# Kernel tuning notes

Measured on AMD Instinct MI355X. Metric: run time of the kernel, lower is better.

## Reference

```python
import jax, jax.numpy as jnp
import numpy as np

BIN_AGG = 16  # binAgg in source
K = 3         # forward-default im2col/col2im kernel size


def _im2col(x, k):
    # torch Im2Col (unfold), pad=0, stride=1, dilation=1
    B, C, H, W = x.shape
    oh, ow = H - k + 1, W - k + 1
    patches = [x[:, :, i:i + oh, j:j + ow] for i in range(k) for j in range(k)]
    cols = jnp.stack(patches, axis=2)            # [B, C, k*k, oh, ow]
    return cols.reshape(B, C * k * k, oh * ow)   # [B, C*k*k, L]


def _col2im(cols, k, H, W):
    # torch Col2Im (fold): overlap-add of patches back to [B, C, H, W]
    B, CK, L = cols.shape
    C = CK // (k * k)
    oh = H - k + 1
    cols = cols.reshape(B, C, k, k, oh, oh)
    img = jnp.zeros((B, C, H, W), cols.dtype)
    for i in range(k):
        for j in range(k):
            img = img.at[:, :, i:i + oh, j:j + oh].add(cols[:, :, i, j])
    return img


def bin_active(x):
    # sign(x) scaled by block-wise mean of |x| over blocks of 16 along last dim
    B, Kd, L = x.shape
    blocks = jnp.abs(x).reshape(B, Kd, L // BIN_AGG, BIN_AGG)
    scale = jnp.mean(blocks, axis=-1, keepdims=True)
    scale = jnp.broadcast_to(scale, blocks.shape).reshape(B, Kd, L)
    return scale * jnp.sign(x)


def setup_inputs() -> dict:
    key = jax.random.key(0)
    ks = jax.random.split(key, 5)
    B, Cin, Cout, H = 8, 64, 128, 130
    x = jax.random.normal(ks[0], (B, Cin, H, H), jnp.float32)
    gamma = 1.0 + 0.1 * jax.random.normal(ks[1], (Cin,), jnp.float32)
    beta = 0.1 * jax.random.normal(ks[2], (Cin,), jnp.float32)
    conv_w = 0.05 * jax.random.normal(ks[3], (Cout, Cin, 3, 3), jnp.float32)
    conv_b = 0.05 * jax.random.normal(ks[4], (Cout,), jnp.float32)
    return {"x": x, "gamma": gamma, "beta": beta, "conv_w": conv_w, "conv_b": conv_b}


def reference(x, gamma, beta, conv_w, conv_b):
    eps = 1e-4  # BatchNorm2d eps in source
    # BatchNorm2d (training-mode batch statistics, affine)
    mean = jnp.mean(x, axis=(0, 2, 3), keepdims=True)
    var = jnp.var(x, axis=(0, 2, 3), keepdims=True)
    xbn = (x - mean) * jax.lax.rsqrt(var + eps) * gamma[None, :, None, None] + beta[None, :, None, None]
    H = x.shape[2]
    cols = _im2col(xbn, K)          # [B, C*9, (H-2)^2]
    cols = bin_active(cols)         # block-mean binary quantization
    img = _col2im(cols, K, H, H)    # [B, C, H, W]
    y = jax.lax.conv_general_dilated(
        img, conv_w, window_strides=(1, 1), padding=((1, 1), (1, 1)),
        dimension_numbers=("NCHW", "OIHW", "NCHW"))
    y = y + conv_b[None, :, None, None]
    return jax.nn.relu(y)
```

## Files before the change

### kernel.cpp

```cpp
#include <hip/hip_runtime.h>
#include <math.h>

#define B_    8
#define CIN   64
#define COUT  128
#define H_    130
#define NPIX  (H_*H_)
#define NPX   (B_*NPIX)
#define IMW   132
#define ROWE  (8*IMW*8)

typedef __attribute__((ext_vector_type(8))) short short8;
typedef __attribute__((ext_vector_type(4))) float f32x4;

__device__ __forceinline__ ushort f2bf(float f) {
    uint u = __builtin_bit_cast(uint, f);
    uint r = (u + 0x7FFFu + ((u >> 16) & 1u)) >> 16;
    return (ushort)r;
}

__global__ __launch_bounds__(256) void bn_stage1(
    const float* __restrict__ x, float* __restrict__ part)
{
    const int c = blockIdx.x, b = blockIdx.y, tid = threadIdx.x;
    const float4* p = (const float4*)(x + ((size_t)b*CIN + c)*NPIX);
    float s = 0.f, q = 0.f;
    for (int i = tid; i < NPIX/4; i += 256) {
        float4 v = p[i];
        s += v.x + v.y + v.z + v.w;
        q += v.x*v.x + v.y*v.y + v.z*v.z + v.w*v.w;
    }
    #pragma unroll
    for (int off = 32; off; off >>= 1) { s += __shfl_down(s, off); q += __shfl_down(q, off); }
    __shared__ float ss[4], qq[4];
    if ((tid & 63) == 0) { ss[tid >> 6] = s; qq[tid >> 6] = q; }
    __syncthreads();
    if (tid == 0) {
        s = ss[0] + ss[1] + ss[2] + ss[3];
        q = qq[0] + qq[1] + qq[2] + qq[3];
        part[(c*B_ + b)*2]     = s;
        part[(c*B_ + b)*2 + 1] = q;
    }
}

__global__ void bn_stage2(
    const float* __restrict__ part, const float* __restrict__ gamma,
    const float* __restrict__ beta, float* __restrict__ abuf, float* __restrict__ bbuf)
{
    int c = threadIdx.x;
    float s = 0.f, q = 0.f;
    for (int b = 0; b < B_; ++b) { s += part[(c*B_+b)*2]; q += part[(c*B_+b)*2+1]; }
    float mean = s * (1.0f/135200.f);
    float var  = q * (1.0f/135200.f) - mean*mean;
    float a = gamma[c] / sqrtf(var + 1e-4f);
    abuf[c] = a;
    bbuf[c] = beta[c] - mean * a;
}

__global__ __launch_bounds__(256) void wprep(
    const float* __restrict__ w, ushort* __restrict__ wT)
{
    int i = blockIdx.x*256 + threadIdx.x;
    int co = i / 576, k = i - co*576;
    int dydx = k >> 6, ci = k & 63;
    wT[i] = f2bf(w[co*576 + ci*9 + dydx]);
}

__global__ __launch_bounds__(256) void binfold(
    const float* __restrict__ x, const float* __restrict__ abuf,
    const float* __restrict__ bbuf, ushort* __restrict__ img)
{
    __shared__ __align__(16) ushort tile[H_*66];
    __shared__ float absrow[4][132];
    __shared__ float wsum[4][24];
    const int yy = blockIdx.x;
    const int b  = blockIdx.y;
    const int tid = threadIdx.x, wv = tid >> 6, lane = tid & 63;
    uint* rowU = (uint*)(img + (size_t)(b*IMW + yy)*ROWE);

    if (yy == 0 || yy == IMW-1) {
        for (int i = tid; i < ROWE/2; i += 256) rowU[i] = 0u;
        return;
    }
    const int y = yy - 1;
    const float county = (float)min(min(y + 1, 3), H_ - y);

    for (int it = 0; it < 16; ++it) {
        const int ci = wv*16 + it;
        const float* row = x + (((size_t)b*CIN + ci)*H_ + y)*H_;
        const float a = abuf[ci], bb = bbuf[ci];
        float v0 = a*row[lane]      + bb;
        float v1 = a*row[lane + 64] + bb;
        float v2 = 0.f;
        if (lane < 2) v2 = a*row[lane + 128] + bb;
        absrow[wv][lane]      = fabsf(v0);
        absrow[wv][lane + 64] = fabsf(v1);
        if (lane < 2) absrow[wv][lane + 128] = fabsf(v2);
        asm volatile("s_waitcnt lgkmcnt(0)" ::: "memory");
        if (lane < 24) {
            int j = lane >> 3, bx = lane & 7;
            int s = j + bx*16;
            float acc = 0.f;
            #pragma unroll
            for (int t = 0; t < 16; ++t) acc += absrow[wv][s + t];
            wsum[wv][j*8 + bx] = acc;
        }
        asm volatile("s_waitcnt lgkmcnt(0)" ::: "memory");
        #pragma unroll
        for (int rep = 0; rep < 3; ++rep) {
            int xp = lane + rep*64;
            if (xp < H_) {
                float v = (rep == 0) ? v0 : (rep == 1) ? v1 : v2;
                float sgn = (v > 0.f) ? 1.f : ((v < 0.f) ? -1.f : 0.f);
                float sum = 0.f;
                #pragma unroll
                for (int j = 0; j < 3; ++j) {
                    int ox = xp - j;
                    if ((unsigned)ox < 128u) sum += wsum[wv][j*8 + (ox >> 4)];
                }
                tile[xp*66 + ci] = f2bf(sgn * county * sum * 0.0625f);
            }
        }
    }
    __syncthreads();
    const uint* tU = (const uint*)tile;
    for (int i = tid; i < 8*H_*4; i += 256) {
        int cg = (int)((unsigned)i / 520u);
        int r  = i - cg*520;
        int xp = r >> 2, u = r & 3;
        rowU[(cg*IMW + xp + 1)*4 + u] = tU[xp*33 + cg*4 + u];
    }
    if (tid < 64) {
        int cg = tid >> 3, side = (tid >> 2) & 1, u = tid & 3;
        rowU[(cg*IMW + (side ? (IMW-1) : 0))*4 + u] = 0u;
    }
}

#define LDSE (3*ROWE + 128)
__global__ __launch_bounds__(256, 3) void conv_mfma(
    const ushort* __restrict__ img, const ushort* __restrict__ wT,
    const float* __restrict__ bias, float* __restrict__ out)
{
    __shared__ __align__(16) ushort sB[LDSE];
    const int y = blockIdx.x, b = blockIdx.y;
    const int tid = threadIdx.x, lane = tid & 63, wv = tid >> 6;
    const int l16 = lane & 15, quad = lane >> 4;
    const int ch = wv >> 1, ph = wv & 1;

    {
        const uint4* src = (const uint4*)(img + (size_t)(b*IMW + y)*ROWE);
        uint4* dst = (uint4*)sB;
        for (int i = tid; i < 3*ROWE/8; i += 256) dst[i] = src[i];
    }
    __syncthreads();

    int wIdx[4];
    #pragma unroll
    for (int mt = 0; mt < 4; ++mt)
        wIdx[mt] = (ch*64 + mt*16 + l16)*576 + quad*8;

    const int ldsLane = (quad*IMW + ph*64 + l16)*8;

    f32x4 acc[4][5];
    #pragma unroll
    for (int mt = 0; mt < 4; ++mt)
        #pragma unroll
        for (int nt = 0; nt < 5; ++nt)
            acc[mt][nt] = (f32x4){0.f, 0.f, 0.f, 0.f};

    #pragma unroll 3
    for (int dydx = 0; dydx < 9; ++dydx) {
        const int dy = (int)((unsigned)dydx / 3u);
        const int dx = dydx - dy*3;
        #pragma unroll
        for (int h = 0; h < 2; ++h) {
            short8 af[4], bf[5];
            #pragma unroll
            for (int mt = 0; mt < 4; ++mt)
                af[mt] = *(const short8*)(wT + wIdx[mt] + dydx*64 + h*32);
            const int koff = dy*ROWE + h*4*IMW*8 + dx*8;
            #pragma unroll
            for (int nt = 0; nt < 5; ++nt)
                bf[nt] = *(const short8*)(sB + ldsLane + koff + nt*16*8);
            #pragma unroll
            for (int mt = 0; mt < 4; ++mt)
                #pragma unroll
                for (int nt = 0; nt < 5; ++nt)
                    acc[mt][nt] = __builtin_amdgcn_mfma_f32_16x16x32_bf16(
                        af[mt], bf[nt], acc[mt][nt], 0, 0, 0);
        }
    }

    const size_t ob = (size_t)b*COUT*NPIX + (size_t)y*H_;
    #pragma unroll
    for (int mt = 0; mt < 4; ++mt) {
        #pragma unroll
        for (int r = 0; r < 4; ++r) {
            const int co = ch*64 + mt*16 + quad*4 + r;
            const float bv = bias[co];
            #pragma unroll
            for (int nt = 0; nt < 5; ++nt) {
                int xq = (ph*4 + nt)*16 + l16;
                if (xq < H_) {
                    float v = acc[mt][nt][r] + bv;
                    out[ob + (size_t)co*NPIX + xq] = v > 0.f ? v : 0.f;
                }
            }
        }
    }
}

extern "C" void kernel_launch(void* const* d_in, const int* in_sizes, int n_in,
                              void* d_out, int out_size, void* d_ws, size_t ws_size,
                              hipStream_t stream)
{
    const float* x      = (const float*)d_in[0];
    const float* gamma  = (const float*)d_in[1];
    const float* beta   = (const float*)d_in[2];
    const float* conv_w = (const float*)d_in[3];
    const float* conv_b = (const float*)d_in[4];
    float* out = (float*)d_out;

    float*  part = (float*)d_ws;
    float*  abuf = part + 1024;
    float*  bbuf = abuf + 64;
    ushort* wT   = (ushort*)(bbuf + 64);
    ushort* img  = wT + 73728;

    bn_stage1<<<dim3(CIN, B_), 256, 0, stream>>>(x, part);
    bn_stage2<<<1, 64, 0, stream>>>(part, gamma, beta, abuf, bbuf);
    wprep<<<288, 256, 0, stream>>>(conv_w, wT);
    binfold<<<dim3(IMW, B_), 256, 0, stream>>>(x, abuf, bbuf, img);
    conv_mfma<<<dim3(H_, B_), 256, 0, stream>>>(img, wT, conv_b, out);
}
```

Before: 194.6 us.

## Split conv rows into half-width tiles and fuse BN finalize into weight prep

The conv kernel now tiles each output row into two 65-pixel halves over a 3D grid. Each block stages only the needed 67-column window (padded to 82) into LDS, and each wave covers 32 output channels across the whole half-row instead of 64 channels by half. This doubles the block count, shrinks LDS and accumulator registers, and raises the occupancy target from 3 to 4, at the cost of reloading the weights once per half. The separate single-block BN finalize launch is also folded into the weight-transpose kernel to save one launch.

New measurement: 184.4 us. 1.05x faster.

```diff
diff --git a/kernel.cpp b/kernel.cpp
--- a/kernel.cpp
+++ b/kernel.cpp
@@ -9,6 +9,7 @@
 #define NPX   (B_*NPIX)
 #define IMW   132
 #define ROWE  (8*IMW*8)
+#define XXS   82
 
 typedef __attribute__((ext_vector_type(8))) short short8;
 typedef __attribute__((ext_vector_type(4))) float f32x4;
@@ -43,27 +44,25 @@
     }
 }
 
-__global__ void bn_stage2(
-    const float* __restrict__ part, const float* __restrict__ gamma,
-    const float* __restrict__ beta, float* __restrict__ abuf, float* __restrict__ bbuf)
-{
-    int c = threadIdx.x;
-    float s = 0.f, q = 0.f;
-    for (int b = 0; b < B_; ++b) { s += part[(c*B_+b)*2]; q += part[(c*B_+b)*2+1]; }
-    float mean = s * (1.0f/135200.f);
-    float var  = q * (1.0f/135200.f) - mean*mean;
-    float a = gamma[c] / sqrtf(var + 1e-4f);
-    abuf[c] = a;
-    bbuf[c] = beta[c] - mean * a;
-}
-
-__global__ __launch_bounds__(256) void wprep(
-    const float* __restrict__ w, ushort* __restrict__ wT)
+__global__ __launch_bounds__(256) void wprep_bn(
+    const float* __restrict__ w, const float* __restrict__ part,
+    const float* __restrict__ gamma, const float* __restrict__ beta,
+    ushort* __restrict__ wT, float* __restrict__ abuf, float* __restrict__ bbuf)
 {
     int i = blockIdx.x*256 + threadIdx.x;
     int co = i / 576, k = i - co*576;
     int dydx = k >> 6, ci = k & 63;
     wT[i] = f2bf(w[co*576 + ci*9 + dydx]);
+    if (blockIdx.x == 0 && threadIdx.x < 64) {
+        int c = threadIdx.x;
+        float s = 0.f, q = 0.f;
+        for (int b = 0; b < B_; ++b) { s += part[(c*B_+b)*2]; q += part[(c*B_+b)*2+1]; }
+        float mean = s * (1.0f/135200.f);
+        float var  = q * (1.0f/135200.f) - mean*mean;
+        float a = gamma[c] / sqrtf(var + 1e-4f);
+        abuf[c] = a;
+        bbuf[c] = beta[c] - mean * a;
+    }
 }
 
 __global__ __launch_bounds__(256) void binfold(
@@ -136,34 +135,42 @@
     }
 }
 
-#define LDSE (3*ROWE + 128)
-__global__ __launch_bounds__(256, 3) void conv_mfma(
+__global__ __launch_bounds__(256, 4) void conv_mfma(
     const ushort* __restrict__ img, const ushort* __restrict__ wT,
     const float* __restrict__ bias, float* __restrict__ out)
 {
-    __shared__ __align__(16) ushort sB[LDSE];
-    const int y = blockIdx.x, b = blockIdx.y;
-    const int tid = threadIdx.x, lane = tid & 63, wv = tid >> 6;
+    __shared__ __align__(16) ushort sB[3*8*XXS*8];
+    const int xh = blockIdx.x, y = blockIdx.y, b = blockIdx.z;
+    const int tid = threadIdx.x, lane = tid & 63, q = tid >> 6;
     const int l16 = lane & 15, quad = lane >> 4;
-    const int ch = wv >> 1, ph = wv & 1;
+    const int x0 = xh * 65;
 
     {
-        const uint4* src = (const uint4*)(img + (size_t)(b*IMW + y)*ROWE);
-        uint4* dst = (uint4*)sB;
-        for (int i = tid; i < 3*ROWE/8; i += 256) dst[i] = src[i];
+        uint4* s4 = (uint4*)sB;
+        const uint4 z = {0u, 0u, 0u, 0u};
+        for (int i = tid; i < 24*XXS; i += 256) {
+            int run = (int)((unsigned)i / (unsigned)XXS);
+            int c   = i - run*XXS;
+            int dy  = run >> 3, cg = run & 7;
+            uint4 v = z;
+            if (c < 67)
+                v = *(const uint4*)(img + (size_t)(b*IMW + y + dy)*ROWE
+                                    + (cg*IMW + x0 + c)*8);
+            s4[run*XXS + c] = v;
+        }
     }
     __syncthreads();
 
-    int wIdx[4];
-    #pragma unroll
-    for (int mt = 0; mt < 4; ++mt)
-        wIdx[mt] = (ch*64 + mt*16 + l16)*576 + quad*8;
-
-    const int ldsLane = (quad*IMW + ph*64 + l16)*8;
-
-    f32x4 acc[4][5];
-    #pragma unroll
-    for (int mt = 0; mt < 4; ++mt)
+    int wIdx[2];
+    #pragma unroll
+    for (int mt = 0; mt < 2; ++mt)
+        wIdx[mt] = (q*32 + mt*16 + l16)*576 + quad*8;
+
+    const int bBase = (quad*XXS + l16)*8;
+
+    f32x4 acc[2][5];
+    #pragma unroll
+    for (int mt = 0; mt < 2; ++mt)
         #pragma unroll
         for (int nt = 0; nt < 5; ++nt)
             acc[mt][nt] = (f32x4){0.f, 0.f, 0.f, 0.f};
@@ -174,16 +181,16 @@
         const int dx = dydx - dy*3;
         #pragma unroll
         for (int h = 0; h < 2; ++h) {
-            short8 af[4], bf[5];
-            #pragma unroll
-            for (int mt = 0; mt < 4; ++mt)
+            short8 af[2], bf[5];
+            #pragma unroll
+            for (int mt = 0; mt < 2; ++mt)
                 af[mt] = *(const short8*)(wT + wIdx[mt] + dydx*64 + h*32);
-            const int koff = dy*ROWE + h*4*IMW*8 + dx*8;
+            const int ko = ((dy*8 + 4*h)*XXS + dx)*8;
             #pragma unroll
             for (int nt = 0; nt < 5; ++nt)
-                bf[nt] = *(const short8*)(sB + ldsLane + koff + nt*16*8);
-            #pragma unroll
-            for (int mt = 0; mt < 4; ++mt)
+                bf[nt] = *(const short8*)(sB + bBase + ko + nt*128);
+            #pragma unroll
+            for (int mt = 0; mt < 2; ++mt)
                 #pragma unroll
                 for (int nt = 0; nt < 5; ++nt)
                     acc[mt][nt] = __builtin_amdgcn_mfma_f32_16x16x32_bf16(
@@ -191,19 +198,19 @@
         }
     }
 
-    const size_t ob = (size_t)b*COUT*NPIX + (size_t)y*H_;
-    #pragma unroll
-    for (int mt = 0; mt < 4; ++mt) {
+    const size_t ob = (size_t)b*COUT*NPIX + (size_t)y*H_ + x0;
+    #pragma unroll
+    for (int mt = 0; mt < 2; ++mt) {
         #pragma unroll
         for (int r = 0; r < 4; ++r) {
-            const int co = ch*64 + mt*16 + quad*4 + r;
+            const int co = q*32 + mt*16 + quad*4 + r;
             const float bv = bias[co];
             #pragma unroll
             for (int nt = 0; nt < 5; ++nt) {
-                int xq = (ph*4 + nt)*16 + l16;
-                if (xq < H_) {
+                int p = nt*16 + l16;
+                if (p < 65) {
                     float v = acc[mt][nt][r] + bv;
-                    out[ob + (size_t)co*NPIX + xq] = v > 0.f ? v : 0.f;
+                    out[ob + (size_t)co*NPIX + p] = v > 0.f ? v : 0.f;
                 }
             }
         }
@@ -228,8 +235,7 @@
     ushort* img  = wT + 73728;
 
     bn_stage1<<<dim3(CIN, B_), 256, 0, stream>>>(x, part);
-    bn_stage2<<<1, 64, 0, stream>>>(part, gamma, beta, abuf, bbuf);
-    wprep<<<288, 256, 0, stream>>>(conv_w, wT);
+    wprep_bn<<<288, 256, 0, stream>>>(conv_w, part, gamma, beta, wT, abuf, bbuf);
     binfold<<<dim3(IMW, B_), 256, 0, stream>>>(x, abuf, bbuf, img);
-    conv_mfma<<<dim3(H_, B_), 256, 0, stream>>>(img, wT, conv_b, out);
-}
+    conv_mfma<<<dim3(2, H_, B_), 256, 0, stream>>>(img, wT, conv_b, out);
+}
```
